# Performance work log

Measured on AMD Instinct MI355X. Metric: run time of the kernel, lower is better.

Reference implementation:

```python
import jax, jax.numpy as jnp
import numpy as np

B_SZ, L_SEQ = 8, 2048
D_MODEL, N_STATE = 1024, 64
NUM_HEADS, N_REC = 1, 8
H_DIM = D_MODEL // NUM_HEADS


def setup_inputs() -> dict:
    key = jax.random.key(0)
    ks = jax.random.split(key, 12)
    Np = N_STATE
    return {
        "u": jax.random.normal(ks[0], (B_SZ, L_SEQ, D_MODEL), jnp.float32),
        "k_proj_w": jax.random.normal(ks[1], (D_MODEL, D_MODEL), jnp.float32) / np.float32(np.sqrt(D_MODEL)),
        "k_proj_b": jax.random.normal(ks[2], (D_MODEL,), jnp.float32) * 0.02,
        "shift_B": jax.random.normal(ks[3], (D_MODEL, Np), jnp.float32) / np.float32(np.sqrt(Np)),
        "shift_C": jax.random.normal(ks[4], (D_MODEL, Np), jnp.float32) / np.float32(np.sqrt(Np)),
        "ssm_k_D": jax.random.normal(ks[5], (D_MODEL,), jnp.float32),
        "log_dt": jax.random.uniform(ks[6], (H_DIM,), jnp.float32, minval=np.float32(np.log(1e-3)), maxval=np.float32(np.log(1e-1))),
        "log_A_real": jnp.log(0.5 * jnp.ones((H_DIM, Np), jnp.float32)),
        "A_imag": jnp.broadcast_to(np.float32(np.pi) * jnp.arange(Np, dtype=jnp.float32), (H_DIM, Np)),
        "B_re": jax.random.normal(ks[7], (H_DIM, Np), jnp.float32),
        "B_im": jax.random.normal(ks[8], (H_DIM, Np), jnp.float32),
    }


def _shift_kernel(Bp, Cp, L):
    # Shift-SSM kernel (SSKernel mode='shift'): K(l) = sum_m C[m+l] * B[m], zero for l >= N.
    N = Bp.shape[-1]
    nfft = 2 * N
    Bf = jnp.fft.rfft(Bp, n=nfft)
    Cf = jnp.fft.rfft(Cp, n=nfft)
    k = jnp.fft.irfft(Cf * jnp.conj(Bf), n=nfft)[..., :N]  # (D, N) linear cross-correlation
    return jnp.pad(k, ((0, 0), (0, L - N)))  # (D, L)


def _kernel_expand(k, log_dt, log_A_real, A_imag, B_re, B_im):
    # Diagonal-SSM state expansion: SSM states x_t = sum_{s<=t} dA^{t-s} dB u_s,
    # read out at N_REC evenly spaced chunk boundaries.
    # k: (B, G, H, L) real -> (B, N_REC, G, H, N) real
    Bb, G, H, L = k.shape
    Lc = L // N_REC
    dt = jnp.exp(log_dt)[:, None]                      # (H,1)
    A = -jnp.exp(log_A_real) + 1j * A_imag             # (H,N)
    dA_log = dt * A                                    # (H,N)
    dB = (B_re + 1j * B_im) * ((jnp.exp(dA_log) - 1.0) / A)  # ZOH discretization
    exps = jnp.arange(Lc - 1, -1, -1, dtype=jnp.float32)      # (Lc,)
    P = jnp.exp(dA_log[..., None] * exps) * dB[..., None]     # (H,N,Lc): dA^{Lc-1-i} dB
    kc = k.reshape(Bb, G, H, N_REC, Lc).astype(P.dtype)
    contrib = jnp.einsum('hnl,bghrl->rbghn', P, kc)           # (N_REC,B,G,H,N)
    dA_Lc = jnp.exp(dA_log * Lc)                              # (H,N)
    x0 = jnp.zeros((Bb, G, H, A.shape[-1]), P.dtype)

    def step(x, c):
        x = dA_Lc * x + c
        return x, x

    _, states = jax.lax.scan(step, x0, contrib)               # (N_REC,B,G,H,N)
    return jnp.transpose(states.real, (1, 0, 2, 3, 4))


def reference(u, k_proj_w, k_proj_b, shift_B, shift_C, ssm_k_D, log_dt, log_A_real, A_imag, B_re, B_im):
    Bb, L, D = u.shape
    # k = W @ u^T + b  -> (B, D, L)
    k = jnp.einsum('bld,hd->bhl', u, k_proj_w) + k_proj_b[None, :, None]
    Ks = _shift_kernel(shift_B, shift_C, L)  # (D, L)
    nfft = 2 * L  # fft_size = L_kernel + L
    conv = jnp.fft.irfft(jnp.fft.rfft(Ks, n=nfft)[None] * jnp.fft.rfft(k, n=nfft), n=nfft)[..., :L]
    k = conv + ssm_k_D[None, :, None] * k
    # rearrange 'b (h d1) l -> b d1 h l'
    k = k.reshape(Bb, H_DIM, NUM_HEADS, L).transpose(0, 2, 1, 3)
    return _kernel_expand(k, log_dt, log_A_real, A_imag, B_re, B_im)
```

## Files before the change

kernel.cpp:

```cpp
#include <hip/hip_runtime.h>
#include <cstddef>
#include <cstdint>

#define L_SEQ 2048
#define DM    1024
#define NREC  8

typedef __attribute__((ext_vector_type(8))) short short8;
typedef __attribute__((ext_vector_type(4))) float f32x4;
typedef __attribute__((ext_vector_type(2))) unsigned int u32x2;

__device__ inline unsigned short f2bf(float f) {
    unsigned u = __float_as_uint(f);
    unsigned r = (u + 0x7FFFu + ((u >> 16) & 1u)) >> 16;
    return (unsigned short)r;
}
__device__ inline float bf2f(unsigned short s) {
    return __uint_as_float(((unsigned)s) << 16);
}
__device__ inline void gload_lds16(const void* g, void* l) {
    __builtin_amdgcn_global_load_lds(
        (const __attribute__((address_space(1))) void*)g,
        (__attribute__((address_space(3))) void*)l, 16, 0, 0);
}
__device__ inline short8 pack8(f32x4 x, f32x4 y) {
    short8 c;
    c[0] = (short)f2bf(x[0]); c[1] = (short)f2bf(x[1]);
    c[2] = (short)f2bf(x[2]); c[3] = (short)f2bf(x[3]);
    c[4] = (short)f2bf(y[0]); c[5] = (short)f2bf(y[1]);
    c[6] = (short)f2bf(y[2]); c[7] = (short)f2bf(y[3]);
    return c;
}

__global__ __launch_bounds__(512, 2) void gemm_fused(
    const float* __restrict__ Wf, const float* __restrict__ uf,
    const float* __restrict__ bias, unsigned short* __restrict__ klin)
{
    __shared__ unsigned short As[2][256 * 32];
    __shared__ unsigned short Bs[2][256 * 32];

    int wg = (int)blockIdx.x;
    wg = (wg & 7) * 32 + (wg >> 3);
    const int b  = wg >> 5;
    const int l0 = ((wg >> 2) & 7) * 256;
    const int h0 = (wg & 3) * 256;
    const int tid = (int)threadIdx.x;
    const int lane = tid & 63, wv = tid >> 6;

    const int sr0  = tid >> 2;
    const int slot = tid & 3;
    const int sr1  = sr0 + 128;
    const float* gA0 = Wf + (size_t)(h0 + sr0) * DM + slot * 8;
    const float* gA1 = Wf + (size_t)(h0 + sr1) * DM + slot * 8;
    const float* gB0 = uf + ((size_t)b * L_SEQ + l0 + sr0) * DM + slot * 8;
    const float* gB1 = uf + ((size_t)b * L_SEQ + l0 + sr1) * DM + slot * 8;
    const int w0off = (sr0 >> 1) * 128 + ((((sr0 & 1) << 2) + slot) ^ ((sr0 >> 1) & 7)) * 16;
    const int w1off = (sr1 >> 1) * 128 + ((((sr1 & 1) << 2) + slot) ^ ((sr1 >> 1) & 7)) * 16;

    const int wm = wv >> 2, wn = wv & 3;
    const int lr = lane & 15, lk = lane >> 4;
    const int foff = (lr >> 1) * 128 + ((((lr & 1) << 2) + lk) ^ (lr >> 1)) * 16;

    f32x4 acc[8][4];
    #pragma unroll
    for (int mf = 0; mf < 8; ++mf)
        #pragma unroll
        for (int nf = 0; nf < 4; ++nf) acc[mf][nf] = (f32x4){0.f, 0.f, 0.f, 0.f};

    {
        f32x4 a0 = *(const f32x4*)(gA0), a1 = *(const f32x4*)(gA0 + 4);
        f32x4 a2 = *(const f32x4*)(gA1), a3 = *(const f32x4*)(gA1 + 4);
        f32x4 b0 = *(const f32x4*)(gB0), b1 = *(const f32x4*)(gB0 + 4);
        f32x4 b2 = *(const f32x4*)(gB1), b3 = *(const f32x4*)(gB1 + 4);
        *(short8*)((char*)&As[0][0] + w0off) = pack8(a0, a1);
        *(short8*)((char*)&As[0][0] + w1off) = pack8(a2, a3);
        *(short8*)((char*)&Bs[0][0] + w0off) = pack8(b0, b1);
        *(short8*)((char*)&Bs[0][0] + w1off) = pack8(b2, b3);
    }
    __syncthreads();

    #pragma unroll 1
    for (int t = 0; t < 32; ++t) {
        const int cur = t & 1;
        const char* Ab = (const char*)&As[cur][0];
        const char* Bb = (const char*)&Bs[cur][0];
        f32x4 a0, a1, a2, a3, b0, b1, b2, b3;
        if (t < 31) {
            const int ko = (t + 1) * 32;
            a0 = *(const f32x4*)(gA0 + ko); a1 = *(const f32x4*)(gA0 + ko + 4);
            a2 = *(const f32x4*)(gA1 + ko); a3 = *(const f32x4*)(gA1 + ko + 4);
            b0 = *(const f32x4*)(gB0 + ko); b1 = *(const f32x4*)(gB0 + ko + 4);
            b2 = *(const f32x4*)(gB1 + ko); b3 = *(const f32x4*)(gB1 + ko + 4);
        }
        short8 af[4], bfr[4];
        #pragma unroll
        for (int nf = 0; nf < 4; ++nf)
            bfr[nf] = *(const short8*)(Bb + (wn * 64 + nf * 16) * 64 + foff);
        #pragma unroll
        for (int mf = 0; mf < 4; ++mf)
            af[mf] = *(const short8*)(Ab + (wm * 128 + mf * 16) * 64 + foff);
        __builtin_amdgcn_s_setprio(1);
        #pragma unroll
        for (int mf = 0; mf < 4; ++mf)
            #pragma unroll
            for (int nf = 0; nf < 4; ++nf)
                acc[mf][nf] = __builtin_amdgcn_mfma_f32_16x16x32_bf16(af[mf], bfr[nf], acc[mf][nf], 0, 0, 0);
        __builtin_amdgcn_s_setprio(0);
        #pragma unroll
        for (int mf = 0; mf < 4; ++mf)
            af[mf] = *(const short8*)(Ab + (wm * 128 + (mf + 4) * 16) * 64 + foff);
        __builtin_amdgcn_s_setprio(1);
        #pragma unroll
        for (int mf = 0; mf < 4; ++mf)
            #pragma unroll
            for (int nf = 0; nf < 4; ++nf)
                acc[mf + 4][nf] = __builtin_amdgcn_mfma_f32_16x16x32_bf16(af[mf], bfr[nf], acc[mf + 4][nf], 0, 0, 0);
        __builtin_amdgcn_s_setprio(0);
        __builtin_amdgcn_sched_barrier(0);
        if (t < 31) {
            char* An = (char*)&As[cur ^ 1][0];
            char* Bn = (char*)&Bs[cur ^ 1][0];
            *(short8*)(An + w0off) = pack8(a0, a1);
            *(short8*)(An + w1off) = pack8(a2, a3);
            *(short8*)(Bn + w0off) = pack8(b0, b1);
            *(short8*)(Bn + w1off) = pack8(b2, b3);
            __syncthreads();
        }
    }

    #pragma unroll
    for (int mf = 0; mf < 8; ++mf) {
        const int h = h0 + wm * 128 + mf * 16 + lk * 4;
        #pragma unroll
        for (int nf = 0; nf < 4; ++nf) {
            const int l = l0 + wn * 64 + nf * 16 + lr;
            #pragma unroll
            for (int r = 0; r < 4; ++r) {
                float v = acc[mf][nf][r] + bias[h + r];
                klin[((size_t)b * DM + h + r) * L_SEQ + l] = f2bf(v);
            }
        }
    }
}

__device__ inline void get_disc(const float* __restrict__ log_dt,
                                const float* __restrict__ lar,
                                const float* __restrict__ aim, int h, int n,
                                float& Are, float& Aim, float& lre, float& lim)
{
    float dtv = expf(log_dt[h]);
    Are = -expf(lar[h * 64 + n]);
    Aim = aim[h * 64 + n];
    lre = dtv * Are;
    lim = dtv * Aim;
}

__global__ __launch_bounds__(256, 5) void expand(
    const unsigned short* __restrict__ klin,
    const float* __restrict__ shift_B, const float* __restrict__ shift_C,
    const float* __restrict__ ssm_k_D, const float* __restrict__ log_dt,
    const float* __restrict__ log_A_real, const float* __restrict__ A_imag,
    const float* __restrict__ B_re, const float* __restrict__ B_im,
    float* __restrict__ out)
{
    __shared__ __align__(16) char sm[29696];
    constexpr int OKL = 0;
    constexpr int OKK = 8704;
    constexpr int OAF = 16896;
    constexpr int OPR = 20224;
    constexpr int OPI = 24320;
    constexpr int OF  = 28416;
    constexpr int OBS = 28672;
    constexpr int OCS = 28928;
    constexpr int OW32 = 29184;

    const int h  = blockIdx.x;
    const int bg = blockIdx.y;
    const int t = threadIdx.x;
    const int lane = t & 63, wv = t >> 6;

    if (t < 32) {
        int rl = t >> 4, reg = (t >> 3) & 1, idx = t & 7;
        *(f32x4*)&sm[OKL + rl * 4352 + reg * 4224 + idx * 16] = (f32x4){0.f, 0.f, 0.f, 0.f};
    }
    {
        const int rl = wv >> 1, hf = wv & 1;
        const int b = bg * 2 + rl;
        const char* krow = (const char*)(klin + ((size_t)b * DM + h) * L_SEQ);
        const int s = (2 * rl + 1 + (lane >> 3)) & 7;
        const int so = hf * 2048 + (lane >> 3) * 128 + ((lane ^ s) & 7) * 16;
        gload_lds16(krow + so,        &sm[OKL + rl * 4352 + 128 + hf * 2048]);
        gload_lds16(krow + so + 1024, &sm[OKL + rl * 4352 + 128 + hf * 2048 + 1024]);
    }
    if (t < 64) {
        ((float*)&sm[OBS])[t] = shift_B[h * 64 + t];
        ((float*)&sm[OCS])[t] = shift_C[h * 64 + t];
        float Are, Aim, lre, lim;
        get_disc(log_dt, log_A_real, A_imag, h, t, Are, Aim, lre, lim);
        float er = expf(32.f * lre);
        float sn, cs; sincosf(32.f * lim, &sn, &cs);
        ((float*)&sm[OW32])[t * 2]     = er * cs;
        ((float*)&sm[OW32])[t * 2 + 1] = er * sn;
    }
    {
        int n = t >> 2, s4 = t & 3;
        float Are, Aim, lre, lim;
        get_disc(log_dt, log_A_real, A_imag, h, n, Are, Aim, lre, lim);
        float erw = expf(lre), snw, csw;
        sincosf(lim, &snw, &csw);
        float wr = erw * csw, wi = erw * snw;
        float e0 = (float)(24 - 8 * s4);
        float mag = expf(e0 * lre);
        float sn0, cs0; sincosf(e0 * lim, &sn0, &cs0);
        float pr = mag * cs0, pi = mag * sn0;
        float vr[8], vi[8];
        vr[7] = pr; vi[7] = pi;
        #pragma unroll
        for (int k = 6; k >= 0; --k) {
            float nr = pr * wr - pi * wi;
            pi = fmaf(pr, wi, pi * wr);
            pr = nr;
            vr[k] = pr; vi[k] = pi;
        }
        short8 re8, im8;
        #pragma unroll
        for (int e = 0; e < 8; ++e) {
            re8[e] = (short)f2bf(vr[e]);
            im8[e] = (short)f2bf(vi[e]);
        }
        *(short8*)&sm[OPR + t * 16] = re8;
        *(short8*)&sm[OPI + t * 16] = im8;
    }
    __syncthreads();

    if (t < 64) {
        const float* Bp = (const float*)&sm[OBS];
        const float* Cp = (const float*)&sm[OCS];
        float f = (t == 0) ? ssm_k_D[h] : 0.f;
        #pragma unroll 8
        for (int j = 0; j < 64; ++j) {
            float cv = Cp[(j + t) & 63];
            f = fmaf((j + t < 64) ? cv : 0.f, Bp[j], f);
        }
        ((float*)&sm[OF])[t] = f;
    }
    __syncthreads();

    {
        int i = t >> 4, ks = t & 15;
        if (ks < 12) {
            const float* Fp = (const float*)&sm[OF];
            short8 row;
            #pragma unroll
            for (int e = 0; e < 8; ++e) {
                int k = ks * 8 + e;
                int m = 64 + i - k;
                float v = (m >= 0 && m < 64) ? Fp[m] : 0.f;
                row[e] = (short)f2bf(v);
            }
            *(short8*)&sm[OAF + i * 208 + ks * 16] = row;
        }
    }
    __syncthreads();

    {
        short8 afr[3];
        #pragma unroll
        for (int ks = 0; ks < 3; ++ks)
            afr[ks] = *(const short8*)&sm[OAF + (lane & 15) * 208 + ks * 64 + (lane >> 4) * 16];
        const int rl = wv >> 1;
        const int jbase = (wv & 1) * 4;
        #pragma unroll
        for (int jj = 0; jj < 4; ++jj) {
            const int jg = jbase + jj;
            f32x4 d = (f32x4){0.f, 0.f, 0.f, 0.f};
            #pragma unroll
            for (int ks = 0; ks < 3; ++ks) {
                int o = rl * 4352 + (jg * 256 + (lane & 15) * 16 + ks * 32 + (lane >> 4) * 8) * 2;
                o ^= ((o >> 7) & 7) << 4;
                short8 bfrag = *(const short8*)&sm[OKL + o];
                d = __builtin_amdgcn_mfma_f32_16x16x32_bf16(afr[ks], bfrag, d, 0, 0, 0);
            }
            unsigned pk0 = ((unsigned)f2bf(d[0])) | (((unsigned)f2bf(d[1])) << 16);
            unsigned pk1 = ((unsigned)f2bf(d[2])) | (((unsigned)f2bf(d[3])) << 16);
            int o2 = rl * 4096 + jg * 512 + (lane & 15) * 32 + (lane >> 4) * 8;
            o2 ^= ((o2 >> 9) & 7) << 4;
            *(u32x2*)&sm[OKK + o2] = (u32x2){pk0, pk1};
        }
    }
    __syncthreads();

    {
        const int mt = wv;
        short8 par = *(const short8*)&sm[OPR + (mt * 16 + (lane & 15)) * 64 + (lane >> 4) * 16];
        short8 pai = *(const short8*)&sm[OPI + (mt * 16 + (lane & 15)) * 64 + (lane >> 4) * 16];
        float w32r[4], w32i[4];
        #pragma unroll
        for (int rg = 0; rg < 4; ++rg) {
            int n = mt * 16 + (lane >> 4) * 4 + rg;
            float2 ww = *(const float2*)&sm[OW32 + n * 8];
            w32r[rg] = ww.x;
            w32i[rg] = ww.y;
        }
        f32x4 cr = (f32x4){0.f, 0.f, 0.f, 0.f};
        f32x4 ci_ = (f32x4){0.f, 0.f, 0.f, 0.f};
        const int colb = (lane & 15) >> 3;
        const int colr = lane & 7;
        #pragma unroll
        for (int g2 = 0; g2 < 8; ++g2) {
            int o = colb * 4096 + colr * 512 + g2 * 64 + (lane >> 4) * 16;
            o ^= ((o >> 9) & 7) << 4;
            short8 kf = *(const short8*)&sm[OKK + o];
            f32x4 sre = __builtin_amdgcn_mfma_f32_16x16x32_bf16(par, kf, (f32x4){0.f,0.f,0.f,0.f}, 0, 0, 0);
            f32x4 sim = __builtin_amdgcn_mfma_f32_16x16x32_bf16(pai, kf, (f32x4){0.f,0.f,0.f,0.f}, 0, 0, 0);
            #pragma unroll
            for (int rg = 0; rg < 4; ++rg) {
                float wr = w32r[rg], wi = w32i[rg];
                float ncr = fmaf(cr[rg], wr, fmaf(-ci_[rg], wi, sre[rg]));
                float nci = fmaf(cr[rg], wi, fmaf(ci_[rg], wr, sim[rg]));
                cr[rg] = ncr;
                ci_[rg] = nci;
            }
        }
        __syncthreads();
        #pragma unroll
        for (int rg = 0; rg < 4; ++rg) {
            int n = mt * 16 + (lane >> 4) * 4 + rg;
            int c = lane & 15;
            ((float*)&sm[OKK])[n * 17 + c] = cr[rg];
            ((float*)&sm[OKK])[1088 + n * 17 + c] = ci_[rg];
        }
    }
    __syncthreads();

    if (t < 128) {
        const int n = t & 63, bl = t >> 6;
        const int b = bg * 2 + bl;
        float Are, Aim, lre, lim;
        get_disc(log_dt, log_A_real, A_imag, h, n, Are, Aim, lre, lim);
        float er = expf(lre), sn, cs;
        sincosf(lim, &sn, &cs);
        float wr = er * cs, wi = er * sn;
        float2 w32v = *(const float2*)&sm[OW32 + n * 8];
        float ar = w32v.x, ai = w32v.y;
        #pragma unroll
        for (int s = 0; s < 3; ++s) {
            float nr = ar * ar - ai * ai;
            ai = 2.f * ar * ai;
            ar = nr;
        }
        float den = Are * Are + Aim * Aim;
        float wm1r = wr - 1.f, wm1i = wi;
        float tr_ = (wm1r * Are + wm1i * Aim) / den;
        float ti_ = (wm1i * Are - wm1r * Aim) / den;
        float br = B_re[h * 64 + n], bi = B_im[h * 64 + n];
        float dBr = br * tr_ - bi * ti_;
        float dBi = br * ti_ + bi * tr_;
        const float* cre = (const float*)&sm[OKK] + n * 17 + bl * 8;
        const float* cim = (const float*)&sm[OKK] + 1088 + n * 17 + bl * 8;
        float sr = 0.f, si_ = 0.f;
        #pragma unroll
        for (int r = 0; r < 8; ++r) {
            float nsr = fmaf(ar, sr, fmaf(-ai, si_, cre[r]));
            float nsi = fmaf(ar, si_, fmaf(ai, sr, cim[r]));
            sr = nsr; si_ = nsi;
            out[(((size_t)b * NREC + r) * DM + h) * 64 + n] = dBr * sr - dBi * si_;
        }
    }
}

extern "C" void kernel_launch(void* const* d_in, const int* in_sizes, int n_in,
                              void* d_out, int out_size, void* d_ws, size_t ws_size,
                              hipStream_t stream)
{
    const float* u       = (const float*)d_in[0];
    const float* W       = (const float*)d_in[1];
    const float* bias    = (const float*)d_in[2];
    const float* shift_B = (const float*)d_in[3];
    const float* shift_C = (const float*)d_in[4];
    const float* ssm_k_D = (const float*)d_in[5];
    const float* log_dt  = (const float*)d_in[6];
    const float* log_Ar  = (const float*)d_in[7];
    const float* A_imag  = (const float*)d_in[8];
    const float* B_re    = (const float*)d_in[9];
    const float* B_im    = (const float*)d_in[10];
    float* out = (float*)d_out;

    unsigned short* klin = (unsigned short*)d_ws;

    gemm_fused<<<dim3(256), 512, 0, stream>>>(W, u, bias, klin);

    expand<<<dim3(DM, 4), 256, 0, stream>>>(klin, shift_B, shift_C, ssm_k_D, log_dt,
                                            log_Ar, A_imag, B_re, B_im, out);
}
```

Measured before the change: 78.16 us.

## Precompute per-channel SSM tables in a separate kernel instead of per expand block

Moves the per-channel discretization, power tables, FIR Toeplitz matrix, w32 and dB computation out of the expand kernel into a new small 'tables' kernel that writes them to workspace. Each expand block, which before redid this work for every batch group, now loads the precomputed bf16 fragments and floats straight from global memory. This removes transcendental math and several barriers from expand and shrinks its LDS footprint, which may raise occupancy. The cost is an extra kernel launch and additional workspace traffic.

```diff
diff --git a/kernel.cpp b/kernel.cpp
--- a/kernel.cpp
+++ b/kernel.cpp
@@ -14,9 +14,6 @@
     unsigned u = __float_as_uint(f);
     unsigned r = (u + 0x7FFFu + ((u >> 16) & 1u)) >> 16;
     return (unsigned short)r;
-}
-__device__ inline float bf2f(unsigned short s) {
-    return __uint_as_float(((unsigned)s) << 16);
 }
 __device__ inline void gload_lds16(const void* g, void* l) {
     __builtin_amdgcn_global_load_lds(
@@ -30,6 +27,101 @@
     c[4] = (short)f2bf(y[0]); c[5] = (short)f2bf(y[1]);
     c[6] = (short)f2bf(y[2]); c[7] = (short)f2bf(y[3]);
     return c;
+}
+__device__ inline void get_disc(const float* __restrict__ log_dt,
+                                const float* __restrict__ lar,
+                                const float* __restrict__ aim, int h, int n,
+                                float& Are, float& Aim, float& lre, float& lim)
+{
+    float dtv = expf(log_dt[h]);
+    Are = -expf(lar[h * 64 + n]);
+    Aim = aim[h * 64 + n];
+    lre = dtv * Are;
+    lim = dtv * Aim;
+}
+
+__global__ __launch_bounds__(512, 2) void tables(
+    const float* __restrict__ shift_B, const float* __restrict__ shift_C,
+    const float* __restrict__ ssm_k_D, const float* __restrict__ log_dt,
+    const float* __restrict__ log_A_real, const float* __restrict__ A_imag,
+    const float* __restrict__ B_re, const float* __restrict__ B_im,
+    unsigned short* __restrict__ Pre_g, unsigned short* __restrict__ Pim_g,
+    unsigned short* __restrict__ Afir_g, float* __restrict__ w32_g,
+    float* __restrict__ dB_g)
+{
+    __shared__ float Fsh[8][64];
+    const int t = (int)threadIdx.x;
+    const int hs = t >> 6, n = t & 63;
+    const int h = (int)blockIdx.x * 8 + hs;
+
+    float Are, Aim, lre, lim;
+    get_disc(log_dt, log_A_real, A_imag, h, n, Are, Aim, lre, lim);
+
+    {
+        float er = expf(32.f * lre), sn, cs;
+        sincosf(32.f * lim, &sn, &cs);
+        ((float2*)w32_g)[h * 64 + n] = make_float2(er * cs, er * sn);
+    }
+    float wr, wi;
+    {
+        float er = expf(lre), sn, cs;
+        sincosf(lim, &sn, &cs);
+        wr = er * cs; wi = er * sn;
+        float den = Are * Are + Aim * Aim;
+        float wm1r = wr - 1.f, wm1i = wi;
+        float tr_ = (wm1r * Are + wm1i * Aim) / den;
+        float ti_ = (wm1i * Are - wm1r * Aim) / den;
+        float br = B_re[h * 64 + n], bi = B_im[h * 64 + n];
+        ((float2*)dB_g)[h * 64 + n] = make_float2(br * tr_ - bi * ti_, br * ti_ + bi * tr_);
+    }
+    {
+        #pragma unroll
+        for (int s4 = 0; s4 < 4; ++s4) {
+            float e0 = (float)(24 - 8 * s4);
+            float mag = expf(e0 * lre), sn0, cs0;
+            sincosf(e0 * lim, &sn0, &cs0);
+            float pr = mag * cs0, pi = mag * sn0;
+            float vr[8], vi[8];
+            vr[7] = pr; vi[7] = pi;
+            #pragma unroll
+            for (int k = 6; k >= 0; --k) {
+                float nr = pr * wr - pi * wi;
+                pi = fmaf(pr, wi, pi * wr);
+                pr = nr;
+                vr[k] = pr; vi[k] = pi;
+            }
+            short8 re8, im8;
+            #pragma unroll
+            for (int e = 0; e < 8; ++e) {
+                re8[e] = (short)f2bf(vr[e]);
+                im8[e] = (short)f2bf(vi[e]);
+            }
+            *(short8*)(Pre_g + (size_t)h * 2048 + n * 32 + s4 * 8) = re8;
+            *(short8*)(Pim_g + (size_t)h * 2048 + n * 32 + s4 * 8) = im8;
+        }
+    }
+    {
+        const float* Bp = shift_B + h * 64;
+        const float* Cp = shift_C + h * 64;
+        float f = (n == 0) ? ssm_k_D[h] : 0.f;
+        for (int j = 0; j + n < 64; ++j) f = fmaf(Cp[j + n], Bp[j], f);
+        Fsh[hs][n] = f;
+    }
+    __syncthreads();
+    {
+        const float* Fp = Fsh[hs];
+        const int i = n >> 2;
+        for (int ks = (n & 3); ks < 12; ks += 4) {
+            short8 row;
+            #pragma unroll
+            for (int e = 0; e < 8; ++e) {
+                int k = ks * 8 + e;
+                int m = 64 + i - k;
+                row[e] = (short)f2bf((m >= 0 && m < 64) ? Fp[m] : 0.f);
+            }
+            *(short8*)(Afir_g + (size_t)h * 1664 + i * 104 + ks * 8) = row;
+        }
+    }
 }
 
 __global__ __launch_bounds__(512, 2) void gemm_fused(
@@ -143,40 +235,19 @@
     }
 }
 
-__device__ inline void get_disc(const float* __restrict__ log_dt,
-                                const float* __restrict__ lar,
-                                const float* __restrict__ aim, int h, int n,
-                                float& Are, float& Aim, float& lre, float& lim)
-{
-    float dtv = expf(log_dt[h]);
-    Are = -expf(lar[h * 64 + n]);
-    Aim = aim[h * 64 + n];
-    lre = dtv * Are;
-    lim = dtv * Aim;
-}
-
 __global__ __launch_bounds__(256, 5) void expand(
     const unsigned short* __restrict__ klin,
-    const float* __restrict__ shift_B, const float* __restrict__ shift_C,
-    const float* __restrict__ ssm_k_D, const float* __restrict__ log_dt,
-    const float* __restrict__ log_A_real, const float* __restrict__ A_imag,
-    const float* __restrict__ B_re, const float* __restrict__ B_im,
-    float* __restrict__ out)
-{
-    __shared__ __align__(16) char sm[29696];
+    const unsigned short* __restrict__ Pre_g, const unsigned short* __restrict__ Pim_g,
+    const unsigned short* __restrict__ Afir_g, const float* __restrict__ w32_g,
+    const float* __restrict__ dB_g, float* __restrict__ out)
+{
+    __shared__ __align__(16) char sm[16896];
     constexpr int OKL = 0;
     constexpr int OKK = 8704;
-    constexpr int OAF = 16896;
-    constexpr int OPR = 20224;
-    constexpr int OPI = 24320;
-    constexpr int OF  = 28416;
-    constexpr int OBS = 28672;
-    constexpr int OCS = 28928;
-    constexpr int OW32 = 29184;
-
-    const int h  = blockIdx.x;
-    const int bg = blockIdx.y;
-    const int t = threadIdx.x;
+
+    const int h  = (int)blockIdx.x;
+    const int bg = (int)blockIdx.y;
+    const int t = (int)threadIdx.x;
     const int lane = t & 63, wv = t >> 6;
 
     if (t < 32) {
@@ -192,82 +263,23 @@
         gload_lds16(krow + so,        &sm[OKL + rl * 4352 + 128 + hf * 2048]);
         gload_lds16(krow + so + 1024, &sm[OKL + rl * 4352 + 128 + hf * 2048 + 1024]);
     }
-    if (t < 64) {
-        ((float*)&sm[OBS])[t] = shift_B[h * 64 + t];
-        ((float*)&sm[OCS])[t] = shift_C[h * 64 + t];
-        float Are, Aim, lre, lim;
-        get_disc(log_dt, log_A_real, A_imag, h, t, Are, Aim, lre, lim);
-        float er = expf(32.f * lre);
-        float sn, cs; sincosf(32.f * lim, &sn, &cs);
-        ((float*)&sm[OW32])[t * 2]     = er * cs;
-        ((float*)&sm[OW32])[t * 2 + 1] = er * sn;
-    }
-    {
-        int n = t >> 2, s4 = t & 3;
-        float Are, Aim, lre, lim;
-        get_disc(log_dt, log_A_real, A_imag, h, n, Are, Aim, lre, lim);
-        float erw = expf(lre), snw, csw;
-        sincosf(lim, &snw, &csw);
-        float wr = erw * csw, wi = erw * snw;
-        float e0 = (float)(24 - 8 * s4);
-        float mag = expf(e0 * lre);
-        float sn0, cs0; sincosf(e0 * lim, &sn0, &cs0);
-        float pr = mag * cs0, pi = mag * sn0;
-        float vr[8], vi[8];
-        vr[7] = pr; vi[7] = pi;
-        #pragma unroll
-        for (int k = 6; k >= 0; --k) {
-            float nr = pr * wr - pi * wi;
-            pi = fmaf(pr, wi, pi * wr);
-            pr = nr;
-            vr[k] = pr; vi[k] = pi;
-        }
-        short8 re8, im8;
-        #pragma unroll
-        for (int e = 0; e < 8; ++e) {
-            re8[e] = (short)f2bf(vr[e]);
-            im8[e] = (short)f2bf(vi[e]);
-        }
-        *(short8*)&sm[OPR + t * 16] = re8;
-        *(short8*)&sm[OPI + t * 16] = im8;
-    }
-    __syncthreads();
-
-    if (t < 64) {
-        const float* Bp = (const float*)&sm[OBS];
-        const float* Cp = (const float*)&sm[OCS];
-        float f = (t == 0) ? ssm_k_D[h] : 0.f;
-        #pragma unroll 8
-        for (int j = 0; j < 64; ++j) {
-            float cv = Cp[(j + t) & 63];
-            f = fmaf((j + t < 64) ? cv : 0.f, Bp[j], f);
-        }
-        ((float*)&sm[OF])[t] = f;
-    }
-    __syncthreads();
-
-    {
-        int i = t >> 4, ks = t & 15;
-        if (ks < 12) {
-            const float* Fp = (const float*)&sm[OF];
-            short8 row;
-            #pragma unroll
-            for (int e = 0; e < 8; ++e) {
-                int k = ks * 8 + e;
-                int m = 64 + i - k;
-                float v = (m >= 0 && m < 64) ? Fp[m] : 0.f;
-                row[e] = (short)f2bf(v);
-            }
-            *(short8*)&sm[OAF + i * 208 + ks * 16] = row;
-        }
-    }
-    __syncthreads();
-
-    {
-        short8 afr[3];
-        #pragma unroll
-        for (int ks = 0; ks < 3; ++ks)
-            afr[ks] = *(const short8*)&sm[OAF + (lane & 15) * 208 + ks * 64 + (lane >> 4) * 16];
+    short8 afr[3];
+    #pragma unroll
+    for (int ks = 0; ks < 3; ++ks)
+        afr[ks] = *(const short8*)(Afir_g + (size_t)h * 1664 + (lane & 15) * 104 + ks * 32 + (lane >> 4) * 8);
+    const int mt = wv;
+    short8 par = *(const short8*)(Pre_g + (size_t)h * 2048 + (mt * 16 + (lane & 15)) * 32 + (lane >> 4) * 8);
+    short8 pai = *(const short8*)(Pim_g + (size_t)h * 2048 + (mt * 16 + (lane & 15)) * 32 + (lane >> 4) * 8);
+    float w32r[4], w32i[4];
+    #pragma unroll
+    for (int rg = 0; rg < 4; ++rg) {
+        int n = mt * 16 + (lane >> 4) * 4 + rg;
+        float2 ww = ((const float2*)w32_g)[h * 64 + n];
+        w32r[rg] = ww.x; w32i[rg] = ww.y;
+    }
+    __syncthreads();
+
+    {
         const int rl = wv >> 1;
         const int jbase = (wv & 1) * 4;
         #pragma unroll
@@ -291,17 +303,6 @@
     __syncthreads();
 
     {
-        const int mt = wv;
-        short8 par = *(const short8*)&sm[OPR + (mt * 16 + (lane & 15)) * 64 + (lane >> 4) * 16];
-        short8 pai = *(const short8*)&sm[OPI + (mt * 16 + (lane & 15)) * 64 + (lane >> 4) * 16];
-        float w32r[4], w32i[4];
-        #pragma unroll
-        for (int rg = 0; rg < 4; ++rg) {
-            int n = mt * 16 + (lane >> 4) * 4 + rg;
-            float2 ww = *(const float2*)&sm[OW32 + n * 8];
-            w32r[rg] = ww.x;
-            w32i[rg] = ww.y;
-        }
         f32x4 cr = (f32x4){0.f, 0.f, 0.f, 0.f};
         f32x4 ci_ = (f32x4){0.f, 0.f, 0.f, 0.f};
         const int colb = (lane & 15) >> 3;
@@ -322,13 +323,12 @@
                 ci_[rg] = nci;
             }
         }
-        __syncthreads();
         #pragma unroll
         for (int rg = 0; rg < 4; ++rg) {
             int n = mt * 16 + (lane >> 4) * 4 + rg;
             int c = lane & 15;
-            ((float*)&sm[OKK])[n * 17 + c] = cr[rg];
-            ((float*)&sm[OKK])[1088 + n * 17 + c] = ci_[rg];
+            ((float*)&sm[OKL])[n * 17 + c] = cr[rg];
+            ((float*)&sm[OKL + 4352])[n * 17 + c] = ci_[rg];
         }
     }
     __syncthreads();
@@ -336,12 +336,7 @@
     if (t < 128) {
         const int n = t & 63, bl = t >> 6;
         const int b = bg * 2 + bl;
-        float Are, Aim, lre, lim;
-        get_disc(log_dt, log_A_real, A_imag, h, n, Are, Aim, lre, lim);
-        float er = expf(lre), sn, cs;
-        sincosf(lim, &sn, &cs);
-        float wr = er * cs, wi = er * sn;
-        float2 w32v = *(const float2*)&sm[OW32 + n * 8];
+        float2 w32v = ((const float2*)w32_g)[h * 64 + n];
         float ar = w32v.x, ai = w32v.y;
         #pragma unroll
         for (int s = 0; s < 3; ++s) {
@@ -349,22 +344,16 @@
             ai = 2.f * ar * ai;
             ar = nr;
         }
-        float den = Are * Are + Aim * Aim;
-        float wm1r = wr - 1.f, wm1i = wi;
-        float tr_ = (wm1r * Are + wm1i * Aim) / den;
-        float ti_ = (wm1i * Are - wm1r * Aim) / den;
-        float br = B_re[h * 64 + n], bi = B_im[h * 64 + n];
-        float dBr = br * tr_ - bi * ti_;
-        float dBi = br * ti_ + bi * tr_;
-        const float* cre = (const float*)&sm[OKK] + n * 17 + bl * 8;
-        const float* cim = (const float*)&sm[OKK] + 1088 + n * 17 + bl * 8;
+        float2 dBv = ((const float2*)dB_g)[h * 64 + n];
+        const float* cre = (const float*)&sm[OKL] + n * 17 + bl * 8;
+        const float* cim = (const float*)&sm[OKL + 4352] + n * 17 + bl * 8;
         float sr = 0.f, si_ = 0.f;
         #pragma unroll
         for (int r = 0; r < 8; ++r) {
             float nsr = fmaf(ar, sr, fmaf(-ai, si_, cre[r]));
             float nsi = fmaf(ar, si_, fmaf(ai, sr, cim[r]));
             sr = nsr; si_ = nsi;
-            out[(((size_t)b * NREC + r) * DM + h) * 64 + n] = dBr * sr - dBi * si_;
+            out[(((size_t)b * NREC + r) * DM + h) * 64 + n] = dBv.x * sr - dBv.y * si_;
         }
     }
 }
@@ -386,10 +375,19 @@
     const float* B_im    = (const float*)d_in[10];
     float* out = (float*)d_out;
 
-    unsigned short* klin = (unsigned short*)d_ws;
+    unsigned short* klin  = (unsigned short*)d_ws;
+    unsigned short* Pre_g = klin + (size_t)8 * L_SEQ * DM;
+    unsigned short* Pim_g = Pre_g + (size_t)DM * 2048;
+    unsigned short* Afir_g = Pim_g + (size_t)DM * 2048;
+    float* w32_g = (float*)(Afir_g + (size_t)DM * 1664);
+    float* dB_g  = w32_g + (size_t)DM * 128;
+
+    tables<<<dim3(128), 512, 0, stream>>>(shift_B, shift_C, ssm_k_D, log_dt,
+                                          log_Ar, A_imag, B_re, B_im,
+                                          Pre_g, Pim_g, Afir_g, w32_g, dB_g);
 
     gemm_fused<<<dim3(256), 512, 0, stream>>>(W, u, bias, klin);
 
-    expand<<<dim3(DM, 4), 256, 0, stream>>>(klin, shift_B, shift_C, ssm_k_D, log_dt,
-                                            log_Ar, A_imag, B_re, B_im, out);
-}
+    expand<<<dim3(DM, 4), 256, 0, stream>>>(klin, Pre_g, Pim_g, Afir_g, w32_g,
+                                            dB_g, out);
+}
```

Result: slower. 82.16 us (+5.1%).
